# Optimization experiments

Measured on AMD Instinct MI355X. Metric: run time of the kernel, lower is better.

## Reference

```python
import jax, jax.numpy as jnp
import numpy as np

B, N, P_EDGE = 2048, 64, 0.08


def setup_inputs() -> dict:
    key = jax.random.key(0)
    k1, _ = jax.random.split(key)
    u = jax.random.uniform(k1, (B, N, N))
    upper = jnp.triu(u < P_EDGE, k=1)
    A = (upper | jnp.swapaxes(upper, -1, -2)).astype(jnp.float32)  # symmetric, zero diag
    E = jnp.stack([1.0 - A, A], axis=-1)  # [B,N,N,2] one-hot edges
    node_mask = jnp.ones((B, N), dtype=jnp.float32)
    return {"E": E, "node_mask": node_mask}


def _diag(X):
    return jnp.diagonal(X, axis1=-2, axis2=-1)


def _trace(X):
    return _diag(X).sum(-1)


def reference(E, node_mask):
    A = E[..., 1:].sum(-1).astype(jnp.float32)  # [B,N,N]
    d = A.sum(-1)                               # degrees [B,N]
    k2 = A @ A
    k3 = k2 @ A
    k4 = k3 @ A
    k5 = k4 @ A
    k6 = k5 @ A

    c3 = _diag(k3)
    k3x = (c3 / 2)[..., None]
    k3y = (c3.sum(-1) / 6)[..., None]

    diag_a4 = _diag(k4)
    c4 = diag_a4 - d * (d - 1) - jnp.einsum('bij,bj->bi', A, d)
    k4x = (c4 / 2)[..., None]
    k4y = (c4.sum(-1) / 8)[..., None]

    diag_a5 = _diag(k5)
    tri = c3
    c5 = diag_a5 - 2 * tri * d - jnp.einsum('bij,bj->bi', A, tri) + tri
    k5x = (c5 / 2)[..., None]
    k5y = (c5.sum(-1) / 10)[..., None]

    t1 = _trace(k6)
    t2 = _trace(k3 ** 2)
    t3 = jnp.sum(A * k2 ** 2, axis=(-2, -1))
    d2 = _diag(k2)
    t4 = (d2 * diag_a4).sum(-1)
    t5 = _trace(k4)
    t6 = _trace(k3)
    t7 = (d2 ** 3).sum(-1)
    t8 = jnp.sum(k3, axis=(-2, -1))
    t9 = (d2 ** 2).sum(-1)
    t10 = _trace(k2)
    c6 = t1 - 3 * t2 + 9 * t3 - 6 * t4 + 6 * t5 - 4 * t6 + 4 * t7 + 3 * t8 - 12 * t9 + 4 * t10
    k6y = (c6 / 12)[..., None]

    x_cycles = jnp.concatenate([k3x, k4x, k5x], axis=-1)            # [B,N,3]
    y_cycles = jnp.concatenate([k3y, k4y, k5y, k6y], axis=-1)       # [B,4]

    x_cycles = x_cycles * node_mask[..., None] / 10.0
    y_cycles = y_cycles / 10.0
    x_cycles = jnp.minimum(x_cycles, 1.0)
    y_cycles = jnp.minimum(y_cycles, 1.0)
    return x_cycles, y_cycles
```

## Files before the change

kernel.cpp:

```cpp
#include <hip/hip_runtime.h>


typedef __attribute__((ext_vector_type(8))) short bf16x8;
typedef __attribute__((ext_vector_type(16))) float f32x16;

constexpr int BATCH = 2048;
constexpr int NN = 64;

__device__ __forceinline__ bf16x8 frag_ld(const unsigned short* buf, int row, int kb2) {
  const int idx = row * 64 + ((kb2 ^ (row & 7)) << 3);
  const uint4 v = *reinterpret_cast<const uint4*>(buf + idx);
  union { uint4 u; bf16x8 b; } cv; cv.u = v; return cv.b;
}

__global__ __launch_bounds__(256, 5) void node_cycle_kernel(
    const float4* __restrict__ E4,
    const float* __restrict__ nmask,
    float* __restrict__ out)
{
  const int b = blockIdx.x;
  const int tid = threadIdx.x;
  const int lane = tid & 63;
  const int w = tid >> 6;
  const int h = lane >> 5;
  const int c31 = lane & 31;
  const int R = w >> 1, C = w & 1;

  __shared__ unsigned short bufA[64 * 64];
  __shared__ unsigned short bufK2[64 * 64];
  __shared__ unsigned short sl[4][64];
  __shared__ uint2 rms[NN];
  __shared__ float c3sh[NN];
  __shared__ float accs[4][7][NN];

  const float4* __restrict__ Eb = E4 + (size_t)b * (NN * NN / 2);

  unsigned mA = 0u, mB = 0u;
  #pragma unroll
  for (int q = 0; q < 8; ++q) {
    const float4 f = Eb[w * 512 + q * 64 + lane];
    const int bit = 2 * q + h;
    mA |= (unsigned)(f.y > 0.5f) << bit;
    mB |= (unsigned)(f.w > 0.5f) << bit;
  }
  mA |= (unsigned)__shfl_xor((int)mA, 32);
  mB |= (unsigned)__shfl_xor((int)mB, 32);
  if (lane < 32) {
    sl[w][2 * lane]     = (unsigned short)mA;
    sl[w][2 * lane + 1] = (unsigned short)mB;
  }
  __syncthreads();

  if (tid < 128) {
    const int c = tid >> 1, hf = tid & 1;
    const unsigned v = (unsigned)sl[2 * hf][c] | ((unsigned)sl[2 * hf + 1][c] << 16);
    if (hf == 0) rms[c].x = v; else rms[c].y = v;
  }
  __syncthreads();

  const uint2 mr = rms[lane];

  {
    const unsigned word = (w < 2) ? mr.x : mr.y;
    const unsigned bits16 = (word >> (16 * (w & 1))) & 0xffffu;
    #pragma unroll
    for (int e = 0; e < 2; ++e) {
      const int bq = 2 * w + e;
      unsigned wv[4];
      #pragma unroll
      for (int p2 = 0; p2 < 4; ++p2) {
        const int c0 = e * 8 + p2 * 2;
        const unsigned b0 = (bits16 >> c0) & 1u;
        const unsigned b1 = (bits16 >> (c0 + 1)) & 1u;
        wv[p2] = (b0 ? 0x3F80u : 0u) | (b1 ? 0x3F800000u : 0u);
      }
      const int idx = lane * 64 + ((bq ^ (lane & 7)) << 3);
      *reinterpret_cast<uint4*>(&bufA[idx]) = make_uint4(wv[0], wv[1], wv[2], wv[3]);
    }
  }
  __syncthreads();

  bf16x8 Af[4], Bf[4];
  #pragma unroll
  for (int K = 0; K < 4; ++K) {
    Af[K] = frag_ld(bufA, R * 32 + c31, 2 * K + h);
    Bf[K] = frag_ld(bufA, C * 32 + c31, 2 * K + h);
  }
  f32x16 acc;
  #pragma unroll
  for (int r = 0; r < 16; ++r) acc[r] = 0.f;
  #pragma unroll
  for (int K = 0; K < 4; ++K)
    acc = __builtin_amdgcn_mfma_f32_32x32x16_bf16(Af[K], Bf[K], acc, 0, 0, 0);

  {
    const int c = C * 32 + c31;
    #pragma unroll
    for (int g = 0; g < 4; ++g) {
      const unsigned w0 = (__float_as_uint(acc[4*g+1]) & 0xffff0000u) |
                          (__float_as_uint(acc[4*g+0]) >> 16);
      const unsigned w1 = (__float_as_uint(acc[4*g+3]) & 0xffff0000u) |
                          (__float_as_uint(acc[4*g+2]) >> 16);
      const int bb = (4 * R + g) ^ (c & 7);
      *reinterpret_cast<uint2*>(&bufK2[c * 64 + bb * 8 + h * 4]) = make_uint2(w0, w1);
    }
  }
  __syncthreads();

  bf16x8 Kf[4];
  #pragma unroll
  for (int K = 0; K < 4; ++K)
    Kf[K] = frag_ld(bufK2, R * 32 + c31, 2 * K + h);
  f32x16 d;
  #pragma unroll
  for (int r = 0; r < 16; ++r) d[r] = 0.f;
  #pragma unroll
  for (int K = 0; K < 4; ++K)
    d = __builtin_amdgcn_mfma_f32_32x32x16_bf16(Kf[K], Bf[K], d, 0, 0, 0);

  if (R == C) {
    const int dtarget = c31 - 4 * h;
    float c3d = 0.f;
    #pragma unroll
    for (int r = 0; r < 16; ++r) {
      const int rowbase = (r & 3) + 8 * (r >> 2);
      c3d += (rowbase == dtarget) ? d[r] : 0.f;
    }
    if (((c31 >> 2) & 1) == h) c3sh[R * 32 + c31] = c3d;
  }

  {
    const int c = C * 32 + c31;
    #pragma unroll
    for (int g = 0; g < 4; ++g) {
      const unsigned u0 = ((unsigned)d[4*g+0]) | (((unsigned)d[4*g+1]) << 16);
      const unsigned u1 = ((unsigned)d[4*g+2]) | (((unsigned)d[4*g+3]) << 16);
      const int bb = (4 * R + g) ^ (c & 7);
      *reinterpret_cast<uint2*>(&bufA[c * 64 + bb * 8 + h * 4]) = make_uint2(u0, u1);
    }
  }
  __syncthreads();

  float diag4 = 0.f, Ad = 0.f, diag5 = 0.f, t3p = 0.f, Atri = 0.f;
  float t1p = 0.f, t8p = 0.f;
  #pragma unroll
  for (int e = 0; e < 2; ++e) {
    const int bq = 2 * w + e;
    const int idx = lane * 64 + ((bq ^ (lane & 7)) << 3);
    const uint4 vk2 = *reinterpret_cast<const uint4*>(&bufK2[idx]);
    const uint4 vk3 = *reinterpret_cast<const uint4*>(&bufA[idx]);
    const float4 c3a = *reinterpret_cast<const float4*>(&c3sh[bq * 8]);
    const float4 c3b = *reinterpret_cast<const float4*>(&c3sh[bq * 8 + 4]);
    const unsigned wk2[4] = {vk2.x, vk2.y, vk2.z, vk2.w};
    const unsigned wk3[4] = {vk3.x, vk3.y, vk3.z, vk3.w};
    const float c3v[8] = {c3a.x, c3a.y, c3a.z, c3a.w, c3b.x, c3b.y, c3b.z, c3b.w};
    #pragma unroll
    for (int e2 = 0; e2 < 4; ++e2) {
      const int j0 = bq * 8 + 2 * e2;
      const float k2lo = __uint_as_float(wk2[e2] << 16);
      const float k2hi = __uint_as_float(wk2[e2] & 0xffff0000u);
      const float k3lo = (float)(wk3[e2] & 0xffffu);
      const float k3hi = (float)(wk3[e2] >> 16);
      diag4 = fmaf(k2lo, k2lo, fmaf(k2hi, k2hi, diag4));
      Ad += k2lo + k2hi;
      diag5 = fmaf(k2lo, k3lo, fmaf(k2hi, k3hi, diag5));
      t1p = fmaf(k3lo, k3lo, fmaf(k3hi, k3hi, t1p));
      t8p += k3lo + k3hi;
      const unsigned b0 = (j0 < 32 ? (mr.x >> j0) : (mr.y >> (j0 - 32))) & 1u;
      const unsigned b1 = ((j0 + 1) < 32 ? (mr.x >> (j0 + 1)) : (mr.y >> (j0 + 1 - 32))) & 1u;
      const float s0 = b0 ? k2lo : 0.f;
      const float s1 = b1 ? k2hi : 0.f;
      t3p = fmaf(s0, k2lo, fmaf(s1, k2hi, t3p));
      Atri += (b0 ? c3v[2 * e2] : 0.f) + (b1 ? c3v[2 * e2 + 1] : 0.f);
    }
  }
  accs[w][0][lane] = diag4;
  accs[w][1][lane] = Ad;
  accs[w][2][lane] = diag5;
  accs[w][3][lane] = t3p;
  accs[w][4][lane] = Atri;
  accs[w][5][lane] = t1p;
  accs[w][6][lane] = t8p;
  __syncthreads();

  if (w == 0) {
    float f[7];
    #pragma unroll
    for (int q2 = 0; q2 < 7; ++q2)
      f[q2] = accs[0][q2][lane] + accs[1][q2][lane]
            + accs[2][q2][lane] + accs[3][q2][lane];
    const float diag4F = f[0], AdF = f[1], d5F = f[2], t3F = f[3],
                AtF = f[4], t1F = f[5], t8F = f[6];
    const float di  = (float)(__popc(mr.x) + __popc(mr.y));
    const float c3i = c3sh[lane];

    const float c4 = diag4F - di * (di - 1.f) - AdF;
    const float c5 = d5F - 2.f * c3i * di - AtF + c3i;
    const float c6p = t1F + 3.f * t8F
              - 3.f * (c3i * c3i)
              + 9.f * t3F
              - 6.f * (di * diag4F)
              + 6.f * diag4F
              - 4.f * c3i
              + 4.f * (di * di * di)
              - 12.f * (di * di)
              + 4.f * di;

    float sc3 = c3i, sc4 = c4, sc5 = c5, sc6 = c6p;
    #pragma unroll
    for (int off = 32; off > 0; off >>= 1) {
      sc3 += __shfl_xor(sc3, off);
      sc4 += __shfl_xor(sc4, off);
      sc5 += __shfl_xor(sc5, off);
      sc6 += __shfl_xor(sc6, off);
    }

    const float m = nmask[b * NN + lane];
    float* xo = out + ((size_t)b * NN + lane) * 3;
    xo[0] = fminf(c3i * 0.5f * m * 0.1f, 1.f);
    xo[1] = fminf(c4 * 0.5f * m * 0.1f, 1.f);
    xo[2] = fminf(c5 * 0.5f * m * 0.1f, 1.f);

    if (lane == 0) {
      float4 y;
      y.x = fminf(sc3 * (1.f / 6.f)  * 0.1f, 1.f);
      y.y = fminf(sc4 * (1.f / 8.f)  * 0.1f, 1.f);
      y.z = fminf(sc5 * (1.f / 10.f) * 0.1f, 1.f);
      y.w = fminf(sc6 * (1.f / 12.f) * 0.1f, 1.f);
      *reinterpret_cast<float4*>(out + (size_t)BATCH * NN * 3 + b * 4) = y;
    }
  }
}

extern "C" void kernel_launch(void* const* d_in, const int* in_sizes, int n_in,
                              void* d_out, int out_size, void* d_ws, size_t ws_size,
                              hipStream_t stream) {
  const float4* E4 = reinterpret_cast<const float4*>(d_in[0]);
  const float* nmask = reinterpret_cast<const float*>(d_in[1]);
  float* out = reinterpret_cast<float*>(d_out);
  node_cycle_kernel<<<BATCH, 256, 0, stream>>>(E4, nmask, out);
}
```

Baseline: 19.30 us.

## Remap final reduction to shuffles, drop shared accumulator buffer, raise occupancy

Changes the per-row reduction mapping so each group of 4 lanes handles one node row. Partial sums are combined with warp shuffles instead of a 7x64 shared-memory staging array read back by a single wave. The epilogue now runs in all four waves, with only a tiny per-wave graph-level partial sum going through shared memory. Fragment loads are interleaved with the MFMAs to shorten register live ranges, and launch bounds are raised from 5 to 8 blocks per CU. The risks are register spilling under the tighter bound and more shuffle instructions.

```diff
diff --git a/kernel.cpp b/kernel.cpp
--- a/kernel.cpp
+++ b/kernel.cpp
@@ -13,7 +13,7 @@
   union { uint4 u; bf16x8 b; } cv; cv.u = v; return cv.b;
 }
 
-__global__ __launch_bounds__(256, 5) void node_cycle_kernel(
+__global__ __launch_bounds__(256, 8) void node_cycle_kernel(
     const float4* __restrict__ E4,
     const float* __restrict__ nmask,
     float* __restrict__ out)
@@ -31,9 +31,13 @@
   __shared__ unsigned short sl[4][64];
   __shared__ uint2 rms[NN];
   __shared__ float c3sh[NN];
-  __shared__ float accs[4][7][NN];
+  __shared__ float4 gpart[4];
 
   const float4* __restrict__ Eb = E4 + (size_t)b * (NN * NN / 2);
+
+  const int rp_r = 16 * w + (lane >> 2);
+  const int rp_q = lane & 3;
+  const float m_r = nmask[b * NN + rp_r];
 
   unsigned mA = 0u, mB = 0u;
   #pragma unroll
@@ -58,10 +62,10 @@
   }
   __syncthreads();
 
-  const uint2 mr = rms[lane];
+  const uint2 mrL = rms[lane];
 
   {
-    const unsigned word = (w < 2) ? mr.x : mr.y;
+    const unsigned word = (w < 2) ? mrL.x : mrL.y;
     const unsigned bits16 = (word >> (16 * (w & 1))) & 0xffffu;
     #pragma unroll
     for (int e = 0; e < 2; ++e) {
@@ -70,9 +74,8 @@
       #pragma unroll
       for (int p2 = 0; p2 < 4; ++p2) {
         const int c0 = e * 8 + p2 * 2;
-        const unsigned b0 = (bits16 >> c0) & 1u;
-        const unsigned b1 = (bits16 >> (c0 + 1)) & 1u;
-        wv[p2] = (b0 ? 0x3F80u : 0u) | (b1 ? 0x3F800000u : 0u);
+        wv[p2] = (((bits16 >> c0) & 1u) ? 0x3F80u : 0u)
+               | (((bits16 >> (c0 + 1)) & 1u) ? 0x3F800000u : 0u);
       }
       const int idx = lane * 64 + ((bq ^ (lane & 7)) << 3);
       *reinterpret_cast<uint4*>(&bufA[idx]) = make_uint4(wv[0], wv[1], wv[2], wv[3]);
@@ -80,18 +83,18 @@
   }
   __syncthreads();
 
-  bf16x8 Af[4], Bf[4];
+  bf16x8 Bf[4];
+  #pragma unroll
+  for (int K = 0; K < 4; ++K) Bf[K] = frag_ld(bufA, C * 32 + c31, 2 * K + h);
+
+  f32x16 acc;
+  #pragma unroll
+  for (int r = 0; r < 16; ++r) acc[r] = 0.f;
   #pragma unroll
   for (int K = 0; K < 4; ++K) {
-    Af[K] = frag_ld(bufA, R * 32 + c31, 2 * K + h);
-    Bf[K] = frag_ld(bufA, C * 32 + c31, 2 * K + h);
-  }
-  f32x16 acc;
-  #pragma unroll
-  for (int r = 0; r < 16; ++r) acc[r] = 0.f;
-  #pragma unroll
-  for (int K = 0; K < 4; ++K)
-    acc = __builtin_amdgcn_mfma_f32_32x32x16_bf16(Af[K], Bf[K], acc, 0, 0, 0);
+    const bf16x8 af = frag_ld(bufA, R * 32 + c31, 2 * K + h);
+    acc = __builtin_amdgcn_mfma_f32_32x32x16_bf16(af, Bf[K], acc, 0, 0, 0);
+  }
 
   {
     const int c = C * 32 + c31;
@@ -107,16 +110,14 @@
   }
   __syncthreads();
 
-  bf16x8 Kf[4];
-  #pragma unroll
-  for (int K = 0; K < 4; ++K)
-    Kf[K] = frag_ld(bufK2, R * 32 + c31, 2 * K + h);
   f32x16 d;
   #pragma unroll
   for (int r = 0; r < 16; ++r) d[r] = 0.f;
   #pragma unroll
-  for (int K = 0; K < 4; ++K)
-    d = __builtin_amdgcn_mfma_f32_32x32x16_bf16(Kf[K], Bf[K], d, 0, 0, 0);
+  for (int K = 0; K < 4; ++K) {
+    const bf16x8 kf = frag_ld(bufK2, R * 32 + c31, 2 * K + h);
+    d = __builtin_amdgcn_mfma_f32_32x32x16_bf16(kf, Bf[K], d, 0, 0, 0);
+  }
 
   if (R == C) {
     const int dtarget = c31 - 4 * h;
@@ -141,12 +142,13 @@
   }
   __syncthreads();
 
+  const uint2 mr = rms[rp_r];
   float diag4 = 0.f, Ad = 0.f, diag5 = 0.f, t3p = 0.f, Atri = 0.f;
   float t1p = 0.f, t8p = 0.f;
   #pragma unroll
   for (int e = 0; e < 2; ++e) {
-    const int bq = 2 * w + e;
-    const int idx = lane * 64 + ((bq ^ (lane & 7)) << 3);
+    const int bq = 2 * rp_q + e;
+    const int idx = rp_r * 64 + ((bq ^ (rp_r & 7)) << 3);
     const uint4 vk2 = *reinterpret_cast<const uint4*>(&bufK2[idx]);
     const uint4 vk3 = *reinterpret_cast<const uint4*>(&bufA[idx]);
     const float4 c3a = *reinterpret_cast<const float4*>(&c3sh[bq * 8]);
@@ -168,67 +170,61 @@
       t8p += k3lo + k3hi;
       const unsigned b0 = (j0 < 32 ? (mr.x >> j0) : (mr.y >> (j0 - 32))) & 1u;
       const unsigned b1 = ((j0 + 1) < 32 ? (mr.x >> (j0 + 1)) : (mr.y >> (j0 + 1 - 32))) & 1u;
-      const float s0 = b0 ? k2lo : 0.f;
-      const float s1 = b1 ? k2hi : 0.f;
-      t3p = fmaf(s0, k2lo, fmaf(s1, k2hi, t3p));
+      t3p = fmaf(b0 ? k2lo : 0.f, k2lo, fmaf(b1 ? k2hi : 0.f, k2hi, t3p));
       Atri += (b0 ? c3v[2 * e2] : 0.f) + (b1 ? c3v[2 * e2 + 1] : 0.f);
     }
   }
-  accs[w][0][lane] = diag4;
-  accs[w][1][lane] = Ad;
-  accs[w][2][lane] = diag5;
-  accs[w][3][lane] = t3p;
-  accs[w][4][lane] = Atri;
-  accs[w][5][lane] = t1p;
-  accs[w][6][lane] = t8p;
-  __syncthreads();
-
-  if (w == 0) {
-    float f[7];
-    #pragma unroll
-    for (int q2 = 0; q2 < 7; ++q2)
-      f[q2] = accs[0][q2][lane] + accs[1][q2][lane]
-            + accs[2][q2][lane] + accs[3][q2][lane];
-    const float diag4F = f[0], AdF = f[1], d5F = f[2], t3F = f[3],
-                AtF = f[4], t1F = f[5], t8F = f[6];
-    const float di  = (float)(__popc(mr.x) + __popc(mr.y));
-    const float c3i = c3sh[lane];
-
-    const float c4 = diag4F - di * (di - 1.f) - AdF;
-    const float c5 = d5F - 2.f * c3i * di - AtF + c3i;
-    const float c6p = t1F + 3.f * t8F
-              - 3.f * (c3i * c3i)
-              + 9.f * t3F
-              - 6.f * (di * diag4F)
-              + 6.f * diag4F
-              - 4.f * c3i
-              + 4.f * (di * di * di)
-              - 12.f * (di * di)
-              + 4.f * di;
-
-    float sc3 = c3i, sc4 = c4, sc5 = c5, sc6 = c6p;
-    #pragma unroll
-    for (int off = 32; off > 0; off >>= 1) {
-      sc3 += __shfl_xor(sc3, off);
-      sc4 += __shfl_xor(sc4, off);
-      sc5 += __shfl_xor(sc5, off);
-      sc6 += __shfl_xor(sc6, off);
-    }
-
-    const float m = nmask[b * NN + lane];
-    float* xo = out + ((size_t)b * NN + lane) * 3;
-    xo[0] = fminf(c3i * 0.5f * m * 0.1f, 1.f);
-    xo[1] = fminf(c4 * 0.5f * m * 0.1f, 1.f);
-    xo[2] = fminf(c5 * 0.5f * m * 0.1f, 1.f);
-
-    if (lane == 0) {
-      float4 y;
-      y.x = fminf(sc3 * (1.f / 6.f)  * 0.1f, 1.f);
-      y.y = fminf(sc4 * (1.f / 8.f)  * 0.1f, 1.f);
-      y.z = fminf(sc5 * (1.f / 10.f) * 0.1f, 1.f);
-      y.w = fminf(sc6 * (1.f / 12.f) * 0.1f, 1.f);
-      *reinterpret_cast<float4*>(out + (size_t)BATCH * NN * 3 + b * 4) = y;
-    }
+  #pragma unroll
+  for (int off = 1; off <= 2; off <<= 1) {
+    diag4 += __shfl_xor(diag4, off);
+    Ad    += __shfl_xor(Ad, off);
+    diag5 += __shfl_xor(diag5, off);
+    t3p   += __shfl_xor(t3p, off);
+    Atri  += __shfl_xor(Atri, off);
+    t1p   += __shfl_xor(t1p, off);
+    t8p   += __shfl_xor(t8p, off);
+  }
+
+  const float di  = (float)(__popc(mr.x) + __popc(mr.y));
+  const float c3i = c3sh[rp_r];
+  const float c4 = diag4 - di * (di - 1.f) - Ad;
+  const float c5 = diag5 - 2.f * c3i * di - Atri + c3i;
+  const float c6p = t1p + 3.f * t8p
+            - 3.f * (c3i * c3i)
+            + 9.f * t3p
+            - 6.f * (di * diag4)
+            + 6.f * diag4
+            - 4.f * c3i
+            + 4.f * (di * di * di)
+            - 12.f * (di * di)
+            + 4.f * di;
+
+  if (rp_q == 0) {
+    float* xo = out + ((size_t)b * NN + rp_r) * 3;
+    xo[0] = fminf(c3i * 0.05f * m_r, 1.f);
+    xo[1] = fminf(c4  * 0.05f * m_r, 1.f);
+    xo[2] = fminf(c5  * 0.05f * m_r, 1.f);
+  }
+
+  float sc3 = c3i, sc4 = c4, sc5 = c5, sc6 = c6p;
+  #pragma unroll
+  for (int off = 4; off < 64; off <<= 1) {
+    sc3 += __shfl_xor(sc3, off);
+    sc4 += __shfl_xor(sc4, off);
+    sc5 += __shfl_xor(sc5, off);
+    sc6 += __shfl_xor(sc6, off);
+  }
+  if (lane == 0) gpart[w] = make_float4(sc3, sc4, sc5, sc6);
+  __syncthreads();
+
+  if (tid == 0) {
+    const float4 g0 = gpart[0], g1 = gpart[1], g2 = gpart[2], g3 = gpart[3];
+    float4 y;
+    y.x = fminf((g0.x + g1.x + g2.x + g3.x) * (1.f / 6.f)  * 0.1f, 1.f);
+    y.y = fminf((g0.y + g1.y + g2.y + g3.y) * (1.f / 8.f)  * 0.1f, 1.f);
+    y.z = fminf((g0.z + g1.z + g2.z + g3.z) * (1.f / 10.f) * 0.1f, 1.f);
+    y.w = fminf((g0.w + g1.w + g2.w + g3.w) * (1.f / 12.f) * 0.1f, 1.f);
+    *reinterpret_cast<float4*>(out + (size_t)BATCH * NN * 3 + b * 4) = y;
   }
 }
 
```

New measurement: 18.81 us, median of 2. 2.6% less time.
